# Kernel tuning notes

Measured on AMD Instinct MI355X. Metric: run time of the kernel, lower is better.

Reference implementation:

```python
import jax, jax.numpy as jnp
import numpy as np

D_MODEL = 1024
D_STATE = 16
D_CONV = 4
EXPAND = 2
D_INNER = D_MODEL * EXPAND
BATCH = 4
SEQLEN = 4096


def setup_inputs() -> dict:
    key = jax.random.key(0)
    ks = jax.random.split(key, 10)
    s = 1.0 / np.sqrt(D_MODEL)
    si = 1.0 / np.sqrt(D_INNER)
    return {
        "x": jax.random.normal(ks[0], (BATCH, SEQLEN, D_MODEL), jnp.float32),
        "x_proj_w": jax.random.normal(ks[1], (D_INNER, D_MODEL), jnp.float32) * s,
        "dt_proj_w": jax.random.normal(ks[2], (D_INNER, D_MODEL), jnp.float32) * s,
        "dt_proj_b": jax.random.normal(ks[3], (D_INNER,), jnp.float32) * 0.1,
        "A_log": jax.random.normal(ks[4], (D_INNER, D_STATE), jnp.float32),
        "D": jnp.ones((D_INNER,), jnp.float32),
        "B_proj_w": jax.random.normal(ks[5], (D_STATE, D_MODEL), jnp.float32) * s,
        "C_proj_w": jax.random.normal(ks[6], (D_STATE, D_MODEL), jnp.float32) * s,
        "conv_w": jax.random.normal(ks[7], (D_INNER, 1, D_CONV), jnp.float32) * 0.5,
        "conv_b": jax.random.normal(ks[8], (D_INNER,), jnp.float32) * 0.1,
        "out_proj_w": jax.random.normal(ks[9], (D_MODEL, D_INNER), jnp.float32) * si,
    }


def _selective_scan(xc, delta, A, B, C, D):
    # xc, delta: (b, L, d_inner); B, C: (b, L, d_state); A: (d_inner, d_state)
    batch, seqlen, d_inner = xc.shape
    d_state = A.shape[1]

    def step(h, inp):
        x_t, dt, B_t, C_t = inp  # (b,di), (b,di), (b,ds), (b,ds)
        A_disc = jnp.exp(dt[:, :, None] * A[None])           # (b, di, ds)
        h = A_disc * h + (dt[:, :, None] * B_t[:, None, :]) * x_t[:, :, None]
        y_t = jnp.einsum('bds,bs->bd', h, C_t) + D[None, :] * x_t
        return h, y_t

    h0 = jnp.zeros((batch, d_inner, d_state), xc.dtype)
    xs = (jnp.swapaxes(xc, 0, 1), jnp.swapaxes(delta, 0, 1),
          jnp.swapaxes(B, 0, 1), jnp.swapaxes(C, 0, 1))
    _, ys = jax.lax.scan(step, h0, xs)  # ys: (L, b, d_inner)
    return jnp.swapaxes(ys, 0, 1)


def reference(x, x_proj_w, dt_proj_w, dt_proj_b, A_log, D, B_proj_w, C_proj_w, conv_w, conv_b, out_proj_w):
    seqlen = x.shape[1]
    x_inner = x @ x_proj_w.T  # (b, L, d_inner)
    # causal depthwise conv1d: torch pads both sides by d_conv-1 then keeps first L,
    # equivalent to left-pad (d_conv-1, 0)
    xc = jax.lax.conv_general_dilated(
        jnp.swapaxes(x_inner, 1, 2), conv_w,
        window_strides=(1,), padding=[(D_CONV - 1, 0)],
        dimension_numbers=('NCH', 'OIH', 'NCH'),
        feature_group_count=D_INNER)
    xc = jnp.swapaxes(xc + conv_b[None, :, None], 1, 2)
    xc = jax.nn.silu(xc)
    B = x @ B_proj_w.T
    C = x @ C_proj_w.T
    delta = jax.nn.softplus(x @ dt_proj_w.T + dt_proj_b)
    A = -jnp.exp(A_log.astype(jnp.float32))
    y = _selective_scan(xc, delta, A, B, C, D)
    return y @ out_proj_w.T
```

## Files before the change

kernel.cpp:

```cpp
#include <hip/hip_runtime.h>
#include <hip/hip_bf16.h>
#include <math.h>

typedef __bf16 bf16;
typedef __bf16 bf16x2 __attribute__((ext_vector_type(2)));
typedef __bf16 bf16x8 __attribute__((ext_vector_type(8)));
typedef float f32x4 __attribute__((ext_vector_type(4)));

#define AS_G __attribute__((address_space(1)))
#define AS_L __attribute__((address_space(3)))

#define NCHUNK 64
#define CLEN   64

__device__ __forceinline__ void async_ld16(const void* g, void* l) {
  __builtin_amdgcn_global_load_lds((const AS_G void*)g, (AS_L void*)l, 16, 0, 0);
}
__device__ __forceinline__ float fexp2(float x) { return __builtin_amdgcn_exp2f(x); }

__global__ void detect_dtype(const void* __restrict__ Dones, int* __restrict__ flag) {
  if (threadIdx.x == 0 && blockIdx.x == 0) {
    *flag = (*(const unsigned int*)Dones == 0x3F803F80u) ? 0 : 1;
  }
}

__global__ __launch_bounds__(256) void to_bf16(
    const void* __restrict__ src, bf16* __restrict__ dst, int n8,
    const int* __restrict__ flag)
{
  const int i = blockIdx.x * 256 + threadIdx.x;
  if (i >= n8) return;
  bf16x8 o;
  if (*flag) {
    const f32x4* s = (const f32x4*)src;
    f32x4 a = s[2*i], b = s[2*i + 1];
    #pragma unroll
    for (int e = 0; e < 4; ++e) { o[e] = (bf16)a[e]; o[e+4] = (bf16)b[e]; }
  } else {
    o = ((const bf16x8*)src)[i];
  }
  ((bf16x8*)dst)[i] = o;
}

template<int EPI>
__global__ __launch_bounds__(512, 2) void gemm_bt2(
    const bf16* __restrict__ A, const bf16* __restrict__ W,
    bf16* __restrict__ OutB, float* __restrict__ OutF,
    const bf16* __restrict__ bias, const int* __restrict__ flag,
    int M, int N, int K)
{
  __shared__ bf16 smA[3][256*32];
  __shared__ bf16 smB[3][256*32];
  const int tid  = threadIdx.x;
  const int wave = tid >> 6;
  const int lane = tid & 63;
  const int bx  = blockIdx.x;
  const int cpx = gridDim.x >> 3;
  const int bxs = (bx & 7) * cpx + (bx >> 3);
  const int m0 = bxs * 256;
  const int n0 = blockIdx.y * 256;
  const int wm = (wave >> 2) * 128;
  const int wn = (wave & 3) * 64;
  const int lm = lane & 15;
  const int q  = lane >> 4;
  const bool f32o = (EPI == 2) && (*flag != 0);

  f32x4 acc[8][4] = {};

  const int c0i = tid;
  const int c1i = tid + 512;
  const int r0 = c0i >> 2, cc0 = c0i & 3;
  const int r1 = c1i >> 2, cc1 = c1i & 3;
  const int sc0 = cc0 ^ ((r0 >> 1) & 3);
  const int sc1 = cc1 ^ ((r1 >> 1) & 3);
  const bf16* gA0 = A + (size_t)(m0 + r0)*K + sc0*8;
  const bf16* gA1 = A + (size_t)(m0 + r1)*K + sc1*8;
  const bf16* gB0 = W + (size_t)(n0 + r0)*K + sc0*8;
  const bf16* gB1 = W + (size_t)(n0 + r1)*K + sc1*8;
  const int o0 = c0i * 8;
  const int o1 = c1i * 8;

  auto stage = [&](int buf, int k0) {
    async_ld16(gA0 + k0, &smA[buf][o0]);
    async_ld16(gA1 + k0, &smA[buf][o1]);
    async_ld16(gB0 + k0, &smB[buf][o0]);
    async_ld16(gB1 + k0, &smB[buf][o1]);
  };

  const int sl = (q ^ ((lm >> 1) & 3)) * 8;

  const int nt = K >> 5;
  stage(0, 0);
  stage(1, 32);

  for (int t = 0; t < nt; ++t) {
    const int buf = t % 3;
    if (t + 2 < nt) {
      stage((t + 2) % 3, (t + 2) * 32);
      asm volatile("s_waitcnt vmcnt(8)" ::: "memory");
    } else if (t + 1 < nt) {
      asm volatile("s_waitcnt vmcnt(4)" ::: "memory");
    } else {
      asm volatile("s_waitcnt vmcnt(0)" ::: "memory");
    }
    __builtin_amdgcn_sched_barrier(0);
    __builtin_amdgcn_s_barrier();
    __builtin_amdgcn_sched_barrier(0);

    const bf16* sA = smA[buf];
    const bf16* sB = smB[buf];
    bf16x8 af[8], bfr[4];
    #pragma unroll
    for (int mi = 0; mi < 8; ++mi)
      af[mi] = *(const bf16x8*)(sA + (wm + mi*16 + lm)*32 + sl);
    #pragma unroll
    for (int ni = 0; ni < 4; ++ni)
      bfr[ni] = *(const bf16x8*)(sB + (wn + ni*16 + lm)*32 + sl);

    __builtin_amdgcn_s_setprio(1);
    #pragma unroll
    for (int mi = 0; mi < 8; ++mi)
      #pragma unroll
      for (int ni = 0; ni < 4; ++ni)
        acc[mi][ni] = __builtin_amdgcn_mfma_f32_16x16x32_bf16(af[mi], bfr[ni], acc[mi][ni], 0, 0, 0);
    __builtin_amdgcn_s_setprio(0);

    asm volatile("s_waitcnt lgkmcnt(0)" ::: "memory");
    __builtin_amdgcn_sched_barrier(0);
    __builtin_amdgcn_s_barrier();
    __builtin_amdgcn_sched_barrier(0);
  }

  #pragma unroll
  for (int mi = 0; mi < 8; ++mi) {
    #pragma unroll
    for (int ni = 0; ni < 4; ++ni) {
      const int col = n0 + wn + ni*16 + lm;
      float bval = 0.f;
      if (EPI == 1) bval = (float)bias[col];
      #pragma unroll
      for (int r = 0; r < 4; ++r) {
        const int row = m0 + wm + mi*16 + q*4 + r;
        float v = acc[mi][ni][r];
        if (EPI == 1) {
          v += bval;
          v = (v > 20.f) ? v : __logf(1.f + __expf(v));
        }
        const size_t idx = (size_t)row*N + col;
        if (EPI == 2 && f32o) OutF[idx] = v;
        else                  OutB[idx] = (bf16)v;
      }
    }
  }
}

__global__ __launch_bounds__(64) void bc_gemm(
    const bf16* __restrict__ X,
    const bf16* __restrict__ Bw, const bf16* __restrict__ Cw,
    float* __restrict__ Bout, float* __restrict__ Cout)
{
  const int lane = threadIdx.x;
  const int lm = lane & 15, q = lane >> 4;
  const int m0 = blockIdx.x * 16;
  const bf16* W = blockIdx.y ? Cw : Bw;
  float* O      = blockIdx.y ? Cout : Bout;
  f32x4 acc = {};
  const bf16* pa = X + (size_t)(m0 + lm)*1024 + q*8;
  const bf16* pw = W + (size_t)lm*1024 + q*8;
  for (int k0 = 0; k0 < 1024; k0 += 32) {
    bf16x8 a = *(const bf16x8*)(pa + k0);
    bf16x8 w = *(const bf16x8*)(pw + k0);
    acc = __builtin_amdgcn_mfma_f32_16x16x32_bf16(a, w, acc, 0, 0, 0);
  }
  #pragma unroll
  for (int r = 0; r < 4; ++r)
    O[(size_t)(m0 + q*4 + r)*16 + lm] = acc[r];
}

__global__ __launch_bounds__(256) void conv_silu(
    const bf16* __restrict__ Xin, const bf16* __restrict__ cw,
    const bf16* __restrict__ cb, bf16* __restrict__ Xc)
{
  const int idx = blockIdx.x * 256 + threadIdx.x;
  const int row = idx >> 8;
  const int dv  = (idx & 255) * 8;
  const int t   = row & 4095;
  bf16x8 wv[4];
  const bf16x8* pw = (const bf16x8*)(cw + (size_t)dv*4);
  #pragma unroll
  for (int j = 0; j < 4; ++j) wv[j] = pw[j];
  bf16x8 bv = *(const bf16x8*)(cb + dv);
  float acc[8];
  #pragma unroll
  for (int e = 0; e < 8; ++e) acc[e] = (float)bv[e];
  #pragma unroll
  for (int j = 0; j < 4; ++j) {
    const int tr = t - 3 + j;
    if (tr < 0) continue;
    bf16x8 xv = *(const bf16x8*)(Xin + (size_t)(row - 3 + j)*2048 + dv);
    #pragma unroll
    for (int e = 0; e < 8; ++e) {
      const int li = e*4 + j;
      acc[e] += (float)xv[e] * (float)wv[li >> 3][li & 7];
    }
  }
  bf16x8 o;
  #pragma unroll
  for (int e = 0; e < 8; ++e) {
    float v = acc[e];
    v = v / (1.f + __expf(-v));
    o[e] = (bf16)v;
  }
  *(bf16x8*)(Xc + (size_t)row*2048 + dv) = o;
}

__global__ __launch_bounds__(256) void scan_phase1(
    const bf16* __restrict__ Xc, const bf16* __restrict__ Dt,
    const float* __restrict__ Bm, const bf16* __restrict__ A_log,
    float* __restrict__ Hend, float* __restrict__ Dtsum)
{
  const int tid = threadIdx.x;
  const int d0 = blockIdx.x * 512 + tid * 2;
  const int c = blockIdx.y;
  const int b = blockIdx.z;
  const int t0 = c * CLEN;
  __shared__ float sB[CLEN*16];
  {
    const f32x4* src = (const f32x4*)(Bm + ((size_t)b*4096 + t0)*16);
    ((f32x4*)sB)[tid] = src[tid];
  }
  __syncthreads();
  float A2[2][16];
  {
    bf16x8 av[4];
    const bf16x8* pA = (const bf16x8*)(A_log + (size_t)d0*16);
    #pragma unroll
    for (int j = 0; j < 4; ++j) av[j] = pA[j];
    #pragma unroll
    for (int u = 0; u < 2; ++u)
      #pragma unroll
      for (int s = 0; s < 16; ++s) {
        const int li = u*16 + s;
        A2[u][s] = -__expf((float)av[li >> 3][li & 7]) * 1.44269504088896f;
      }
  }
  float h[2][16] = {};
  float dts[2] = {0.f, 0.f};
  const bf16* pX = Xc + ((size_t)b*4096 + t0)*2048 + d0;
  const bf16* pD = Dt + ((size_t)b*4096 + t0)*2048 + d0;
  bf16x2 vD = *(const bf16x2*)pD;
  bf16x2 vX = *(const bf16x2*)pX;
  for (int t = 0; t < CLEN; ++t) {
    bf16x2 nD = vD, nX = vX;
    if (t < CLEN-1) {
      nD = *(const bf16x2*)(pD + (size_t)(t+1)*2048);
      nX = *(const bf16x2*)(pX + (size_t)(t+1)*2048);
    }
    f32x4 Bv[4];
    #pragma unroll
    for (int i = 0; i < 4; ++i) Bv[i] = ((const f32x4*)(sB + t*16))[i];
    #pragma unroll
    for (int u = 0; u < 2; ++u) {
      const float dt = (float)vD[u];
      const float xv = (float)vX[u];
      dts[u] += dt;
      const float dx = dt * xv;
      #pragma unroll
      for (int s = 0; s < 16; ++s) {
        const float ad = fexp2(dt * A2[u][s]);
        h[u][s] = ad*h[u][s] + dx * Bv[s>>2][s&3];
      }
    }
    vD = nD; vX = nX;
  }
  #pragma unroll
  for (int u = 0; u < 2; ++u) {
    const size_t base = (((size_t)b*NCHUNK + c)*2048 + d0 + u)*16;
    #pragma unroll
    for (int s = 0; s < 16; ++s) Hend[base + s] = h[u][s];
    Dtsum[((size_t)b*NCHUNK + c)*2048 + d0 + u] = dts[u];
  }
}

__global__ __launch_bounds__(256) void scan_phase2(
    float* __restrict__ H,
    const float* __restrict__ Dtsum,
    const bf16* __restrict__ A_log)
{
  const int idx = blockIdx.x*256 + threadIdx.x;
  const int s = idx & 15;
  const int d = (idx >> 4) & 2047;
  const int b = idx >> 15;
  const float A2 = -__expf((float)A_log[d*16 + s]) * 1.44269504088896f;
  float h = 0.f;
  for (int c = 0; c < NCHUNK; ++c) {
    const size_t off = (((size_t)b*NCHUNK + c)*2048 + d)*16 + s;
    const float hend = H[off];
    H[off] = h;
    const float ap = fexp2(A2 * Dtsum[((size_t)b*NCHUNK + c)*2048 + d]);
    h = h*ap + hend;
  }
}

__global__ __launch_bounds__(256) void scan_phase3(
    const bf16* __restrict__ Xc, const bf16* __restrict__ Dt,
    const float* __restrict__ Bm, const float* __restrict__ Cm,
    const bf16* __restrict__ A_log, const bf16* __restrict__ Dvec,
    const float* __restrict__ Hstart, bf16* __restrict__ Y)
{
  const int tid = threadIdx.x;
  const int d0 = blockIdx.x * 512 + tid * 2;
  const int c = blockIdx.y;
  const int b = blockIdx.z;
  const int t0 = c * CLEN;
  __shared__ float sB[CLEN*16];
  __shared__ float sC[CLEN*16];
  {
    const f32x4* srcB = (const f32x4*)(Bm + ((size_t)b*4096 + t0)*16);
    const f32x4* srcC = (const f32x4*)(Cm + ((size_t)b*4096 + t0)*16);
    ((f32x4*)sB)[tid] = srcB[tid];
    ((f32x4*)sC)[tid] = srcC[tid];
  }
  __syncthreads();
  float A2[2][16];
  {
    bf16x8 av[4];
    const bf16x8* pA = (const bf16x8*)(A_log + (size_t)d0*16);
    #pragma unroll
    for (int j = 0; j < 4; ++j) av[j] = pA[j];
    #pragma unroll
    for (int u = 0; u < 2; ++u)
      #pragma unroll
      for (int s = 0; s < 16; ++s) {
        const int li = u*16 + s;
        A2[u][s] = -__expf((float)av[li >> 3][li & 7]) * 1.44269504088896f;
      }
  }
  float h[2][16];
  #pragma unroll
  for (int u = 0; u < 2; ++u) {
    const size_t base = (((size_t)b*NCHUNK + c)*2048 + d0 + u)*16;
    #pragma unroll
    for (int s = 0; s < 16; ++s) h[u][s] = Hstart[base + s];
  }
  const float Dd0 = (float)Dvec[d0];
  const float Dd1 = (float)Dvec[d0 + 1];
  const bf16* pX = Xc + ((size_t)b*4096 + t0)*2048 + d0;
  const bf16* pD = Dt + ((size_t)b*4096 + t0)*2048 + d0;
  bf16*       pY = Y  + ((size_t)b*4096 + t0)*2048 + d0;
  bf16x2 vD = *(const bf16x2*)pD;
  bf16x2 vX = *(const bf16x2*)pX;
  for (int t = 0; t < CLEN; ++t) {
    bf16x2 nD = vD, nX = vX;
    if (t < CLEN-1) {
      nD = *(const bf16x2*)(pD + (size_t)(t+1)*2048);
      nX = *(const bf16x2*)(pX + (size_t)(t+1)*2048);
    }
    f32x4 Bv[4], Cv[4];
    #pragma unroll
    for (int i = 0; i < 4; ++i) {
      Bv[i] = ((const f32x4*)(sB + t*16))[i];
      Cv[i] = ((const f32x4*)(sC + t*16))[i];
    }
    float y[2];
    #pragma unroll
    for (int u = 0; u < 2; ++u) {
      const float dt = (float)vD[u];
      const float xv = (float)vX[u];
      const float dx = dt * xv;
      float yp[4] = {0.f, 0.f, 0.f, 0.f};
      #pragma unroll
      for (int s = 0; s < 16; ++s) {
        const float ad = fexp2(dt * A2[u][s]);
        h[u][s] = ad*h[u][s] + dx * Bv[s>>2][s&3];
        yp[s & 3] += h[u][s] * Cv[s>>2][s&3];
      }
      y[u] = ((yp[0] + yp[1]) + (yp[2] + yp[3])) + (u ? Dd1 : Dd0) * xv;
    }
    bf16x2 yo; yo[0] = (bf16)y[0]; yo[1] = (bf16)y[1];
    *(bf16x2*)(pY + (size_t)t*2048) = yo;
    vD = nD; vX = nX;
  }
}

extern "C" void kernel_launch(void* const* d_in, const int* in_sizes, int n_in,
                              void* d_out, int out_size, void* d_ws, size_t ws_size,
                              hipStream_t stream)
{
  char* ws = (char*)d_ws;
  size_t off = 0;
  auto alloc = [&](size_t bytes) -> char* {
    char* p = ws + off; off += (bytes + 255) & ~(size_t)255; return p;
  };
  bf16*  xin = (bf16*) alloc((size_t)16384*2048*2);
  bf16*  dlt = (bf16*) alloc((size_t)16384*2048*2);
  bf16*  xc  = (bf16*) alloc((size_t)16384*2048*2);
  float* Bm  = (float*)alloc((size_t)16384*16*4);
  float* Cm  = (float*)alloc((size_t)16384*16*4);
  int*   flag = (int*) alloc(256);
  const int ncanon = 11;
  static const int canon_n[11] = {
    4*4096*1024, 2048*1024, 2048*1024, 2048, 2048*16, 2048,
    16*1024, 16*1024, 2048*4, 2048, 1024*2048 };
  bf16* canon[11];
  for (int i = 0; i < ncanon; ++i) canon[i] = (bf16*)alloc((size_t)canon_n[i]*2);
  float* Hst = (float*)canon[0];
  float* Dts = (float*)canon[1];
  if (off > ws_size) return;

  detect_dtype<<<1, 64, 0, stream>>>(d_in[5], flag);
  for (int i = 0; i < ncanon; ++i) {
    const int n8 = canon_n[i] / 8;
    to_bf16<<<(n8 + 255)/256, 256, 0, stream>>>(d_in[i], canon[i], n8, flag);
  }
  const bf16* x          = canon[0];
  const bf16* x_proj_w   = canon[1];
  const bf16* dt_proj_w  = canon[2];
  const bf16* dt_proj_b  = canon[3];
  const bf16* A_log      = canon[4];
  const bf16* Dvec       = canon[5];
  const bf16* B_proj_w   = canon[6];
  const bf16* C_proj_w   = canon[7];
  const bf16* conv_w     = canon[8];
  const bf16* conv_b     = canon[9];
  const bf16* out_proj_w = canon[10];

  gemm_bt2<0><<<dim3(64,8), 512, 0, stream>>>(x, x_proj_w,  xin, nullptr, nullptr,   flag, 16384, 2048, 1024);
  gemm_bt2<1><<<dim3(64,8), 512, 0, stream>>>(x, dt_proj_w, dlt, nullptr, dt_proj_b, flag, 16384, 2048, 1024);
  bc_gemm<<<dim3(1024,2), 64, 0, stream>>>(x, B_proj_w, C_proj_w, Bm, Cm);
  conv_silu<<<dim3(16384), 256, 0, stream>>>(xin, conv_w, conv_b, xc);
  scan_phase1<<<dim3(4,NCHUNK,4), 256, 0, stream>>>(xc, dlt, Bm, A_log, Hst, Dts);
  scan_phase2<<<dim3(512),        256, 0, stream>>>(Hst, Dts, A_log);
  scan_phase3<<<dim3(4,NCHUNK,4), 256, 0, stream>>>(xc, dlt, Bm, Cm, A_log, Dvec, Hst, xin );
  gemm_bt2<2><<<dim3(64,4), 512, 0, stream>>>(xin, out_proj_w, (bf16*)d_out, (float*)d_out, nullptr, flag, 16384, 1024, 2048);
}
```

Measured before the change: 675.6 us.

## Restructure bf16 GEMM into four-phase K=64 double-buffered pipeline

Replaces the three-stage, 32-wide K pipeline in the projection GEMMs with a two-buffer scheme over 64-wide K tiles. Each tile is split into four phases that interleave the async global-to-LDS loads for the next tile with MFMA work on half of the A rows. The aim is finer-grained overlap of memory traffic and matrix math, with smaller per-phase register fragments. In exchange it uses more LDS (128KB instead of 96KB), adds more barriers and waits per K step, and relies on a hand-tuned vmcnt count being correct.

```diff
diff --git a/kernel.cpp b/kernel.cpp
--- a/kernel.cpp
+++ b/kernel.cpp
@@ -43,20 +43,19 @@
 }
 
 template<int EPI>
-__global__ __launch_bounds__(512, 2) void gemm_bt2(
+__global__ __launch_bounds__(512, 2) void gemm8p(
     const bf16* __restrict__ A, const bf16* __restrict__ W,
     bf16* __restrict__ OutB, float* __restrict__ OutF,
     const bf16* __restrict__ bias, const int* __restrict__ flag,
     int M, int N, int K)
 {
-  __shared__ bf16 smA[3][256*32];
-  __shared__ bf16 smB[3][256*32];
+  __shared__ bf16 smA[2][2][256*32];
+  __shared__ bf16 smB[2][2][256*32];
   const int tid  = threadIdx.x;
   const int wave = tid >> 6;
   const int lane = tid & 63;
-  const int bx  = blockIdx.x;
   const int cpx = gridDim.x >> 3;
-  const int bxs = (bx & 7) * cpx + (bx >> 3);
+  const int bxs = (blockIdx.x & 7) * cpx + (blockIdx.x >> 3);
   const int m0 = bxs * 256;
   const int n0 = blockIdx.y * 256;
   const int wm = (wave >> 2) * 128;
@@ -67,68 +66,77 @@
 
   f32x4 acc[8][4] = {};
 
-  const int c0i = tid;
-  const int c1i = tid + 512;
-  const int r0 = c0i >> 2, cc0 = c0i & 3;
-  const int r1 = c1i >> 2, cc1 = c1i & 3;
-  const int sc0 = cc0 ^ ((r0 >> 1) & 3);
-  const int sc1 = cc1 ^ ((r1 >> 1) & 3);
+  const int r0 = tid >> 2,         c0 = tid & 3;
+  const int r1 = (tid + 512) >> 2, c1 = (tid + 512) & 3;
+  const int sc0 = c0 ^ ((r0 >> 1) & 3);
+  const int sc1 = c1 ^ ((r1 >> 1) & 3);
   const bf16* gA0 = A + (size_t)(m0 + r0)*K + sc0*8;
   const bf16* gA1 = A + (size_t)(m0 + r1)*K + sc1*8;
   const bf16* gB0 = W + (size_t)(n0 + r0)*K + sc0*8;
   const bf16* gB1 = W + (size_t)(n0 + r1)*K + sc1*8;
-  const int o0 = c0i * 8;
-  const int o1 = c1i * 8;
-
-  auto stage = [&](int buf, int k0) {
-    async_ld16(gA0 + k0, &smA[buf][o0]);
-    async_ld16(gA1 + k0, &smA[buf][o1]);
-    async_ld16(gB0 + k0, &smB[buf][o0]);
-    async_ld16(gB1 + k0, &smB[buf][o1]);
+  const int o0 = tid * 8;
+  const int o1 = (tid + 512) * 8;
+
+  auto stageQ = [&](int t, int ph) {
+    const int buf = t & 1;
+    const int kh  = ph >> 1;
+    const int kofs = t*64 + kh*32;
+    if (ph & 1) {
+      async_ld16(gB0 + kofs, &smB[buf][kh][o0]);
+      async_ld16(gB1 + kofs, &smB[buf][kh][o1]);
+    } else {
+      async_ld16(gA0 + kofs, &smA[buf][kh][o0]);
+      async_ld16(gA1 + kofs, &smA[buf][kh][o1]);
+    }
   };
 
   const int sl = (q ^ ((lm >> 1) & 3)) * 8;
 
-  const int nt = K >> 5;
-  stage(0, 0);
-  stage(1, 32);
+  const int nt = K >> 6;
+
+  stageQ(0, 0); stageQ(0, 1); stageQ(0, 2); stageQ(0, 3);
 
   for (int t = 0; t < nt; ++t) {
-    const int buf = t % 3;
-    if (t + 2 < nt) {
-      stage((t + 2) % 3, (t + 2) * 32);
-      asm volatile("s_waitcnt vmcnt(8)" ::: "memory");
-    } else if (t + 1 < nt) {
-      asm volatile("s_waitcnt vmcnt(4)" ::: "memory");
-    } else {
-      asm volatile("s_waitcnt vmcnt(0)" ::: "memory");
-    }
-    __builtin_amdgcn_sched_barrier(0);
-    __builtin_amdgcn_s_barrier();
-    __builtin_amdgcn_sched_barrier(0);
-
-    const bf16* sA = smA[buf];
-    const bf16* sB = smB[buf];
-    bf16x8 af[8], bfr[4];
-    #pragma unroll
-    for (int mi = 0; mi < 8; ++mi)
-      af[mi] = *(const bf16x8*)(sA + (wm + mi*16 + lm)*32 + sl);
-    #pragma unroll
-    for (int ni = 0; ni < 4; ++ni)
-      bfr[ni] = *(const bf16x8*)(sB + (wn + ni*16 + lm)*32 + sl);
-
-    __builtin_amdgcn_s_setprio(1);
-    #pragma unroll
-    for (int mi = 0; mi < 8; ++mi)
-      #pragma unroll
-      for (int ni = 0; ni < 4; ++ni)
-        acc[mi][ni] = __builtin_amdgcn_mfma_f32_16x16x32_bf16(af[mi], bfr[ni], acc[mi][ni], 0, 0, 0);
-    __builtin_amdgcn_s_setprio(0);
-
-    asm volatile("s_waitcnt lgkmcnt(0)" ::: "memory");
-    __builtin_amdgcn_sched_barrier(0);
-    __builtin_amdgcn_s_barrier();
-    __builtin_amdgcn_sched_barrier(0);
+    const int buf = t & 1;
+    const bool pre = (t + 1 < nt);
+    bf16x8 bfr[4];
+    #pragma unroll
+    for (int ph = 0; ph < 4; ++ph) {
+      const int kh  = ph >> 1;
+      const int chh = ph & 1;
+      if (pre) {
+        stageQ(t + 1, ph);
+        asm volatile("s_waitcnt vmcnt(6)" ::: "memory");
+      } else {
+        asm volatile("s_waitcnt vmcnt(0)" ::: "memory");
+      }
+      __builtin_amdgcn_sched_barrier(0);
+      __builtin_amdgcn_s_barrier();
+      __builtin_amdgcn_sched_barrier(0);
+
+      const bf16* sA = &smA[buf][kh][0];
+      if (chh == 0) {
+        const bf16* sB = &smB[buf][kh][0];
+        #pragma unroll
+        for (int ni = 0; ni < 4; ++ni)
+          bfr[ni] = *(const bf16x8*)(sB + (wn + ni*16 + lm)*32 + sl);
+      }
+      bf16x8 af[4];
+      #pragma unroll
+      for (int mi = 0; mi < 4; ++mi)
+        af[mi] = *(const bf16x8*)(sA + (wm + chh*64 + mi*16 + lm)*32 + sl);
+
+      asm volatile("s_waitcnt lgkmcnt(0)" ::: "memory");
+      __builtin_amdgcn_sched_barrier(0);
+      __builtin_amdgcn_s_setprio(1);
+      #pragma unroll
+      for (int mi = 0; mi < 4; ++mi)
+        #pragma unroll
+        for (int ni = 0; ni < 4; ++ni)
+          acc[chh*4 + mi][ni] =
+            __builtin_amdgcn_mfma_f32_16x16x32_bf16(af[mi], bfr[ni], acc[chh*4 + mi][ni], 0, 0, 0);
+      __builtin_amdgcn_s_setprio(0);
+    }
   }
 
   #pragma unroll
@@ -425,12 +433,12 @@
   const bf16* conv_b     = canon[9];
   const bf16* out_proj_w = canon[10];
 
-  gemm_bt2<0><<<dim3(64,8), 512, 0, stream>>>(x, x_proj_w,  xin, nullptr, nullptr,   flag, 16384, 2048, 1024);
-  gemm_bt2<1><<<dim3(64,8), 512, 0, stream>>>(x, dt_proj_w, dlt, nullptr, dt_proj_b, flag, 16384, 2048, 1024);
+  gemm8p<0><<<dim3(64,8), 512, 0, stream>>>(x, x_proj_w,  xin, nullptr, nullptr,   flag, 16384, 2048, 1024);
+  gemm8p<1><<<dim3(64,8), 512, 0, stream>>>(x, dt_proj_w, dlt, nullptr, dt_proj_b, flag, 16384, 2048, 1024);
   bc_gemm<<<dim3(1024,2), 64, 0, stream>>>(x, B_proj_w, C_proj_w, Bm, Cm);
   conv_silu<<<dim3(16384), 256, 0, stream>>>(xin, conv_w, conv_b, xc);
   scan_phase1<<<dim3(4,NCHUNK,4), 256, 0, stream>>>(xc, dlt, Bm, A_log, Hst, Dts);
   scan_phase2<<<dim3(512),        256, 0, stream>>>(Hst, Dts, A_log);
   scan_phase3<<<dim3(4,NCHUNK,4), 256, 0, stream>>>(xc, dlt, Bm, Cm, A_log, Dvec, Hst, xin );
-  gemm_bt2<2><<<dim3(64,4), 512, 0, stream>>>(xin, out_proj_w, (bf16*)d_out, (float*)d_out, nullptr, flag, 16384, 1024, 2048);
-}
+  gemm8p<2><<<dim3(64,4), 512, 0, stream>>>(xin, out_proj_w, (bf16*)d_out, (float*)d_out, nullptr, flag, 16384, 1024, 2048);
+}
```

After: 634.8 us. 6.0% less time.
